# Kernel optimization log

Measured on AMD Instinct MI355X. Metric: run time of the kernel, lower is better.

## Reference

```python
import jax, jax.numpy as jnp
import numpy as np
from math import factorial, sqrt

LMAX = 2
NB = 32
NRBF = 20
CUTOFF = 5.0
N_ATOMS = 20000
N_EDGES = 400000
T = 2
M = (LMAX + 1) ** 2
LIDX = np.repeat(np.arange(LMAX + 1), 2 * np.arange(LMAX + 1) + 1)  # l of each flat (l,m) index


def _cg_complex(j1, m1, j2, m2, j3, m3):
    # Racah formula for complex-SH Clebsch-Gordan coefficients
    if m3 != m1 + m2 or j3 < abs(j1 - j2) or j3 > j1 + j2:
        return 0.0
    f = factorial
    pref = sqrt((2 * j3 + 1) * f(j1 + j2 - j3) * f(j1 - j2 + j3) * f(-j1 + j2 + j3) / f(j1 + j2 + j3 + 1))
    pref *= sqrt(f(j1 + m1) * f(j1 - m1) * f(j2 + m2) * f(j2 - m2) * f(j3 + m3) * f(j3 - m3))
    kmin = max(0, j2 - j3 - m1, j1 + m2 - j3)
    kmax = min(j1 + j2 - j3, j1 - m1, j2 + m2)
    s = 0.0
    for k in range(kmin, kmax + 1):
        s += (-1) ** k / (f(k) * f(j1 + j2 - j3 - k) * f(j1 - m1 - k) * f(j2 + m2 - k) * f(j3 - j2 + m1 + k) * f(j3 - j1 - m2 + k))
    return pref * s


def _u_matrix(l):
    # real-SH = U @ complex-SH (rows: real m from -l..l, cols: complex m')
    U = np.zeros((2 * l + 1, 2 * l + 1), dtype=np.complex128)
    for m in range(-l, l + 1):
        if m == 0:
            U[l, l] = 1.0
        elif m > 0:
            U[l + m, l + m] = (-1) ** m / sqrt(2)
            U[l + m, l - m] = 1.0 / sqrt(2)
        else:
            mu = -m
            U[l + m, l + m] = 1j / sqrt(2)
            U[l + m, l - m] = -1j * (-1) ** mu / sqrt(2)
    return U


def _build_cg_rsh(lmax):
    # CG coefficients in the real-SH basis, parity invariant (odd l1+l2+l3 blocks zero)
    cg = np.zeros((M, M, M), dtype=np.float64)
    Us = [_u_matrix(l) for l in range(lmax + 1)]
    for l1 in range(lmax + 1):
        for l2 in range(lmax + 1):
            for l3 in range(lmax + 1):
                if (l1 + l2 + l3) % 2 == 1 or l3 < abs(l1 - l2) or l3 > l1 + l2:
                    continue
                Cc = np.zeros((2 * l1 + 1, 2 * l2 + 1, 2 * l3 + 1), dtype=np.complex128)
                for i, m1 in enumerate(range(-l1, l1 + 1)):
                    for j, m2 in enumerate(range(-l2, l2 + 1)):
                        m3 = m1 + m2
                        if abs(m3) <= l3:
                            Cc[i, j, l3 + m3] = _cg_complex(l1, m1, l2, m2, l3, m3)
                R = np.einsum('ai,bj,ck,ijk->abc', Us[l1], Us[l2], np.conj(Us[l3]), Cc)
                cg[l1 * l1:(l1 + 1) ** 2, l2 * l2:(l2 + 1) ** 2, l3 * l3:(l3 + 1) ** 2] = np.real(R)
    return cg.astype(np.float32)


CG = jnp.asarray(_build_cg_rsh(LMAX))   # [9, 9, 9]
LIDX_J = jnp.asarray(LIDX)


def _rsh(dirs):
    # real spherical harmonics up to l=2 on unit vectors, flat (l,m) order -> [P, 9]
    x, y, z = dirs[:, 0], dirs[:, 1], dirs[:, 2]
    c1 = 0.4886025119029199
    c2 = 1.0925484305920792
    return jnp.stack([
        jnp.full_like(x, 0.28209479177387814),
        c1 * y, c1 * z, c1 * x,
        c2 * x * y, c2 * y * z,
        0.31539156525252005 * (3.0 * z * z - 1.0),
        c2 * x * z,
        0.5462742152960396 * (x * x - y * y),
    ], axis=1)


def _forward(atomic_numbers, r_ij, idx_i, idx_j, emb, Wf, bf, Wm1, Wm2, Wm3, Wg, bg):
    d = jnp.linalg.norm(r_ij, axis=1)                      # [P]
    Y = _rsh(r_ij / d[:, None])                            # [P, 9]
    offsets = jnp.linspace(0.0, CUTOFF, NRBF)
    width = CUTOFF / (NRBF - 1)
    radial = jnp.exp(-0.5 / width ** 2 * (d[:, None] - offsets) ** 2)   # GaussianRBF [P, NRBF]
    fcut = jnp.where(d < CUTOFF, 0.5 * (jnp.cos(d * jnp.pi / CUTOFF) + 1.0), 0.0)  # CosineCutoff
    x0 = emb[atomic_numbers]                               # nuclear embedding [N, NB]
    x = jnp.concatenate([x0[:, None, :], jnp.zeros((x0.shape[0], M - 1, NB), x0.dtype)], axis=1)  # scalar2rsh
    for t in range(T):
        # SO3Convolution: per-edge radial filter per output degree l, cutoff gated
        Wl = ((radial @ Wf[t].T + bf[t]) * fcut[:, None]).reshape(-1, LMAX + 1, NB)
        xj = x[idx_j]                                      # gather neighbors [P, 9, NB]
        tbc = jnp.einsum('pa,abc->pbc', Y, CG)             # contract Y_ij with CG
        yij = jnp.einsum('pbc,pbn->pcn', tbc, xj) * Wl[:, LIDX_J, :]
        dx = jax.ops.segment_sum(yij, idx_i, num_segments=x.shape[0], indices_are_sorted=True)
        ddx = jnp.einsum('xcn,kn->xck', dx, Wm1[t])        # mixing1 (no bias)
        dx = dx + jnp.einsum('abc,xan,xbn->xcn', CG, dx, ddx)  # SO3TensorProduct
        dx = jnp.einsum('xcn,kn->xck', dx, Wm2[t])         # mixing2
        h = jax.nn.sigmoid((dx[:, 0, :] @ Wg[t].T + bg[t]).reshape(-1, LMAX + 1, NB))
        dx = dx * h[:, LIDX_J, :]                          # SO3ParametricGatedNonlinearity
        dx = jnp.einsum('xcn,kn->xck', dx, Wm3[t])         # mixing3
        x = x + dx
    return x                                               # multipole representation [N, 9, NB]


def setup_inputs():
    key = jax.random.key(0)
    ks = jax.random.split(key, 12)
    return {
        'atomic_numbers': jax.random.randint(ks[0], (N_ATOMS,), 1, 100),
        'r_ij': jax.random.normal(ks[1], (N_EDGES, 3), jnp.float32),
        'idx_i': jnp.sort(jax.random.randint(ks[2], (N_EDGES,), 0, N_ATOMS)),
        'idx_j': jax.random.randint(ks[3], (N_EDGES,), 0, N_ATOMS),
        'emb': jax.random.normal(ks[4], (101, NB), jnp.float32).at[0].set(0.0),
        'Wf': jax.random.normal(ks[5], (T, (LMAX + 1) * NB, NRBF), jnp.float32) / sqrt(NRBF),
        'bf': jnp.zeros((T, (LMAX + 1) * NB), jnp.float32),
        'Wm1': jax.random.normal(ks[6], (T, NB, NB), jnp.float32) / sqrt(NB),
        'Wm2': jax.random.normal(ks[7], (T, NB, NB), jnp.float32) / sqrt(NB),
        'Wm3': jax.random.normal(ks[8], (T, NB, NB), jnp.float32) / sqrt(NB),
        'Wg': jax.random.normal(ks[9], (T, (LMAX + 1) * NB, NB), jnp.float32) / sqrt(NB),
        'bg': jnp.zeros((T, (LMAX + 1) * NB), jnp.float32),
    }


def reference(atomic_numbers, r_ij, idx_i, idx_j, emb, Wf, bf, Wm1, Wm2, Wm3, Wg, bg):
    return _forward(atomic_numbers, r_ij, idx_i, idx_j, emb, Wf, bf, Wm1, Wm2, Wm3, Wg, bg)
```

## Files before the change

### kernel.cpp

```cpp
#include <hip/hip_runtime.h>

#define CHUNK 16

constexpr double CFACT[8] = {1.,1.,2.,6.,24.,120.,720.,5040.};

constexpr double csqrt(double x){
  if (x <= 0.0) return 0.0;
  double s = 1.0;
  while (x > 4.0)  { x *= 0.25; s *= 2.0; }
  while (x < 0.25) { x *= 4.0;  s *= 0.5; }
  double g = 1.0;
  for (int i=0;i<10;i++) g = 0.5*(g + x/g);
  return s*g;
}

constexpr double cg_complex(int j1,int m1,int j2,int m2,int j3,int m3){
  if (m3 != m1+m2 || j3 < (j1>j2?j1-j2:j2-j1) || j3 > j1+j2) return 0.0;
  double pref = csqrt((2.0*j3+1.0)*CFACT[j1+j2-j3]*CFACT[j1-j2+j3]*CFACT[-j1+j2+j3]/CFACT[j1+j2+j3+1]);
  pref *= csqrt(CFACT[j1+m1]*CFACT[j1-m1]*CFACT[j2+m2]*CFACT[j2-m2]*CFACT[j3+m3]*CFACT[j3-m3]);
  int kmin = 0;
  if (j2-j3-m1 > kmin) kmin = j2-j3-m1;
  if (j1+m2-j3 > kmin) kmin = j1+m2-j3;
  int kmax = j1+j2-j3;
  if (j1-m1 < kmax) kmax = j1-m1;
  if (j2+m2 < kmax) kmax = j2+m2;
  double s = 0.0;
  for (int k=kmin;k<=kmax;++k){
    double t = 1.0/(CFACT[k]*CFACT[j1+j2-j3-k]*CFACT[j1-m1-k]*CFACT[j2+m2-k]*CFACT[j3-j2+m1+k]*CFACT[j3-j1-m2+k]);
    s += (k&1)? -t : t;
  }
  return pref*s;
}

struct UR { int n; int mc[2]; double re[2]; double im[2]; };
constexpr UR u_row(int m){
  UR u{}; const double is2 = 0.70710678118654752440;
  if (m==0){ u.n=1; u.mc[0]=0; u.re[0]=1.0; u.im[0]=0.0; u.mc[1]=0; u.re[1]=0.0; u.im[1]=0.0; }
  else if (m>0){ u.n=2; u.mc[0]=m;  u.re[0]=((m&1)? -is2:is2); u.im[0]=0.0;
                        u.mc[1]=-m; u.re[1]=is2;               u.im[1]=0.0; }
  else { int mu=-m; u.n=2; u.mc[0]=m;  u.re[0]=0.0; u.im[0]=is2;
                           u.mc[1]=mu; u.re[1]=0.0; u.im[1]=((mu&1)? is2:-is2); }
  return u;
}

struct CGTab { float v[9][9][9]; };
constexpr CGTab build_cg(){
  CGTab g{};
  double cc[9][9][9] = {};
  for (int a=0;a<9;a++){
    int l1 = (a==0)?0:((a<4)?1:2); int m1 = a - (l1*l1+l1);
    for (int b=0;b<9;b++){
      int l2 = (b==0)?0:((b<4)?1:2); int m2 = b - (l2*l2+l2);
      int m3 = m1+m2;
      for (int l3=0;l3<=2;l3++){
        if (m3 < -l3 || m3 > l3) continue;
        cc[a][b][l3*l3+l3+m3] = cg_complex(l1,m1,l2,m2,l3,m3);
      }
    }
  }
  for (int l1=0;l1<=2;l1++) for (int l2=0;l2<=2;l2++) for (int l3=0;l3<=2;l3++){
    if (((l1+l2+l3)&1)==1) continue;
    int dl = (l1>l2)?(l1-l2):(l2-l1);
    if (l3 < dl || l3 > l1+l2) continue;
    for (int m1=-l1;m1<=l1;m1++) for (int m2=-l2;m2<=l2;m2++) for (int m3=-l3;m3<=l3;m3++){
      UR ua = u_row(m1), ub = u_row(m2), uc = u_row(m3);
      double acc = 0.0;
      for (int i=0;i<ua.n;i++) for (int j=0;j<ub.n;j++){
        double zr = ua.re[i]*ub.re[j] - ua.im[i]*ub.im[j];
        double zi = ua.re[i]*ub.im[j] + ua.im[i]*ub.re[j];
        for (int k=0;k<uc.n;k++){
          double rp = zr*uc.re[k] + zi*uc.im[k];
          if (rp != 0.0)
            acc += rp * cc[l1*l1+l1+ua.mc[i]][l2*l2+l2+ub.mc[j]][l3*l3+l3+uc.mc[k]];
        }
      }
      g.v[l1*l1+l1+m1][l2*l2+l2+m2][l3*l3+l3+m3] = (float)acc;
    }
  }
  return g;
}
constexpr CGTab CGT = build_cg();

__device__ __forceinline__ int swizzle_block(int b, int nb){
  int P = nb >> 3;
  if (b < (P<<3)) return (b & 7) * P + (b >> 3);
  return b;
}

template<bool FIRST>
__global__ __launch_bounds__(256) void edge_kernel(
    const float* __restrict__ r_ij, const int* __restrict__ idx_i, const int* __restrict__ idx_j,
    const float* __restrict__ x, const int* __restrict__ Z, const float* __restrict__ emb,
    const float* __restrict__ Wf_t, const float* __restrict__ bf_t,
    float* __restrict__ dx, int n_edges)
{
  int tid = threadIdx.x;
  int g = tid >> 5, lane = tid & 31;

  int vb = swizzle_block(blockIdx.x, gridDim.x);
  int base = (vb*8 + g)*CHUNK;
  if (base >= n_edges) return;

  int pidx;
  {
    int e0 = base + (lane & 15);
    if (e0 > n_edges-1) e0 = n_edges-1;
    pidx = (lane < 16) ? idx_i[e0] : idx_j[e0];
  }
  float rv0, rv1;
  {
    long long rmax = (long long)n_edges*3 - 1;
    long long a0 = (long long)base*3 + lane;       if (a0 > rmax) a0 = rmax;
    long long a1 = (long long)base*3 + 32 + lane;  if (a1 > rmax) a1 = rmax;
    rv0 = r_ij[a0];
    rv1 = r_ij[a1];
  }

  float wfr[3][20]; float bfl[3];
  #pragma unroll
  for (int l=0;l<3;l++){
    const float* rp = Wf_t + (l*32+lane)*20;
    #pragma unroll
    for (int q=0;q<5;q++){
      float4 v4 = *reinterpret_cast<const float4*>(rp + q*4);
      wfr[l][q*4+0]=v4.x; wfr[l][q*4+1]=v4.y; wfr[l][q*4+2]=v4.z; wfr[l][q*4+3]=v4.w;
    }
    bfl[l] = bf_t[l*32+lane];
  }

  const float STEP  = 5.0f/19.0f;
  const float ALPHA = -0.5f/(STEP*STEP);
  float myoff = (float)lane * STEP;

  float racc[9];
  #pragma unroll
  for (int c=0;c<9;c++) racc[c]=0.f;
  int cur_i = -1;

  float xjn[9]; float xjn0;
  {
    int j0 = __shfl(pidx, 16, 32);
    if (FIRST){
      xjn0 = emb[Z[j0]*32 + lane];
    } else {
      const float* xp = x + j0*288 + lane;
      #pragma unroll
      for (int b=0;b<9;b++) xjn[b] = xp[b*32];
    }
  }

  #pragma unroll
  for (int k=0;k<CHUNK;k++){
    int e = base + k;
    if (e >= n_edges) break;

    float xj[9]; float xj0;
    if (FIRST){
      xj0 = xjn0;
    } else {
      #pragma unroll
      for (int b=0;b<9;b++) xj[b] = xjn[b];
    }

    if (k+1 < CHUNK){
      int jn = __shfl(pidx, 16+k+1, 32);
      if (FIRST){
        xjn0 = emb[Z[jn]*32 + lane];
      } else {
        const float* xp = x + jn*288 + lane;
        #pragma unroll
        for (int b=0;b<9;b++) xjn[b] = xp[b*32];
      }
    }

    int ii = __shfl(pidx, k, 32);

    float rx = (3*k+0 < 32) ? __shfl(rv0, 3*k+0, 32) : __shfl(rv1, 3*k+0-32, 32);
    float ry = (3*k+1 < 32) ? __shfl(rv0, 3*k+1, 32) : __shfl(rv1, 3*k+1-32, 32);
    float rz = (3*k+2 < 32) ? __shfl(rv0, 3*k+2, 32) : __shfl(rv1, 3*k+2-32, 32);

    float d2 = fmaf(rx,rx,fmaf(ry,ry,rz*rz));
    float dd = sqrtf(d2);
    float inv = __fdividef(1.0f, dd);
    float X = rx*inv, Yv = ry*inv, Zv = rz*inv;
    const float c1 = 0.4886025119029199f, c2 = 1.0925484305920792f;
    float Y[9];
    Y[0]=0.28209479177387814f; Y[1]=c1*Yv; Y[2]=c1*Zv; Y[3]=c1*X;
    Y[4]=c2*X*Yv; Y[5]=c2*Yv*Zv; Y[6]=0.31539156525252005f*(3.f*Zv*Zv-1.f);
    Y[7]=c2*X*Zv; Y[8]=0.5462742152960396f*(X*X-Yv*Yv);

    float dtl = dd - myoff;
    float rbl = __expf(ALPHA*dtl*dtl);
    float wl0=bfl[0], wl1=bfl[1], wl2=bfl[2];
    #pragma unroll
    for (int r=0;r<20;r++){
      float rb = __shfl(rbl, r, 32);
      wl0 = fmaf(rb, wfr[0][r], wl0);
      wl1 = fmaf(rb, wfr[1][r], wl1);
      wl2 = fmaf(rb, wfr[2][r], wl2);
    }
    float fc = (dd < 5.0f) ? 0.5f*(__cosf(dd*0.6283185307179586f)+1.0f) : 0.0f;
    wl0*=fc; wl1*=fc; wl2*=fc;

    if (ii != cur_i){
      if (cur_i >= 0){
        float* dp = dx + cur_i*288 + lane;
        #pragma unroll
        for (int c=0;c<9;c++){ atomicAdd(dp + c*32, racc[c]); racc[c]=0.f; }
      }
      cur_i = ii;
    }

    if (FIRST){
      racc[0] = fmaf(wl0, Y[0]*xj0, racc[0]);
      #pragma unroll
      for (int c=1;c<4;c++) racc[c] = fmaf(wl1, Y[c]*xj0, racc[c]);
      #pragma unroll
      for (int c=4;c<9;c++) racc[c] = fmaf(wl2, Y[c]*xj0, racc[c]);
    } else {
      float yv[9];
      #pragma unroll
      for (int c=0;c<9;c++) yv[c]=0.f;
      #pragma unroll
      for (int a=0;a<9;a++){
        #pragma unroll
        for (int b=0;b<9;b++){
          bool any = false;
          #pragma unroll
          for (int c=0;c<9;c++) any = any | (CGT.v[a][b][c] != 0.f);
          if (any){
            float p = Y[a]*xj[b];
            #pragma unroll
            for (int c=0;c<9;c++){
              if (CGT.v[a][b][c] != 0.f) yv[c] = fmaf(CGT.v[a][b][c], p, yv[c]);
            }
          }
        }
      }
      racc[0] = fmaf(wl0, yv[0], racc[0]);
      #pragma unroll
      for (int c=1;c<4;c++) racc[c] = fmaf(wl1, yv[c], racc[c]);
      #pragma unroll
      for (int c=4;c<9;c++) racc[c] = fmaf(wl2, yv[c], racc[c]);
    }
  }
  if (cur_i >= 0){
    float* dp = dx + cur_i*288 + lane;
    #pragma unroll
    for (int c=0;c<9;c++) atomicAdd(dp + c*32, racc[c]);
  }
}

template<bool FIRST, bool LAST>
__global__ __launch_bounds__(256) void atom_kernel(
    float* __restrict__ x, float* __restrict__ dxg,
    const int* __restrict__ Z, const float* __restrict__ emb,
    const float* __restrict__ Wm1_t, const float* __restrict__ Wm2_t, const float* __restrict__ Wm3_t,
    const float* __restrict__ Wg_t, const float* __restrict__ bg_t, int n_atoms)
{
  __shared__ __align__(16) float tile[8][288];
  int tid = threadIdx.x;
  int g = tid>>5, k = tid&31;
  int vb = swizzle_block(blockIdx.x, gridDim.x);
  int atom = vb*8 + g;
  if (atom >= n_atoms) return;
  float* tg = &tile[g][0];
  const float4* t4 = reinterpret_cast<const float4*>(tg);

  float embv;
  if (FIRST) embv = emb[Z[atom]*32 + k];

  float* dp = dxg + atom*288 + k;
  float v[9];
  #pragma unroll
  for (int c=0;c<9;c++){
    v[c]=dp[c*32]; tg[c*32+k]=v[c];
    if (!LAST) dp[c*32]=0.f;
  }

  float wr[32];
  {
    const float4* w4 = reinterpret_cast<const float4*>(Wm1_t + k*32);
    #pragma unroll
    for (int q=0;q<8;q++){ float4 a=w4[q]; wr[4*q]=a.x; wr[4*q+1]=a.y; wr[4*q+2]=a.z; wr[4*q+3]=a.w; }
  }
  float u[9];
  #pragma unroll
  for (int c=0;c<9;c++){
    float s=0.f;
    #pragma unroll
    for (int q=0;q<8;q++){
      float4 tv = t4[c*8+q];
      s = fmaf(tv.x, wr[4*q+0], s); s = fmaf(tv.y, wr[4*q+1], s);
      s = fmaf(tv.z, wr[4*q+2], s); s = fmaf(tv.w, wr[4*q+3], s);
    }
    u[c]=s;
  }

  float w[9];
  #pragma unroll
  for (int c=0;c<9;c++) w[c]=v[c];
  #pragma unroll
  for (int a=0;a<9;a++){
    #pragma unroll
    for (int b=0;b<9;b++){
      bool any = false;
      #pragma unroll
      for (int c=0;c<9;c++) any = any | (CGT.v[a][b][c] != 0.f);
      if (any){
        float p = v[a]*u[b];
        #pragma unroll
        for (int c=0;c<9;c++){
          if (CGT.v[a][b][c] != 0.f) w[c] = fmaf(CGT.v[a][b][c], p, w[c]);
        }
      }
    }
  }

  #pragma unroll
  for (int c=0;c<9;c++) tg[c*32+k]=w[c];
  {
    const float4* w4 = reinterpret_cast<const float4*>(Wm2_t + k*32);
    #pragma unroll
    for (int q=0;q<8;q++){ float4 a=w4[q]; wr[4*q]=a.x; wr[4*q+1]=a.y; wr[4*q+2]=a.z; wr[4*q+3]=a.w; }
  }
  float p[9];
  #pragma unroll
  for (int c=0;c<9;c++){
    float s=0.f;
    #pragma unroll
    for (int q=0;q<8;q++){
      float4 tv = t4[c*8+q];
      s = fmaf(tv.x, wr[4*q+0], s); s = fmaf(tv.y, wr[4*q+1], s);
      s = fmaf(tv.z, wr[4*q+2], s); s = fmaf(tv.w, wr[4*q+3], s);
    }
    p[c]=s;
  }

  tg[k] = p[0];
  float s0=bg_t[k], s1=bg_t[32+k], s2=bg_t[64+k];
  {
    const float4* wg0 = reinterpret_cast<const float4*>(Wg_t + (     k)*32);
    const float4* wg1 = reinterpret_cast<const float4*>(Wg_t + (32 + k)*32);
    const float4* wg2 = reinterpret_cast<const float4*>(Wg_t + (64 + k)*32);
    #pragma unroll
    for (int q=0;q<8;q++){
      float4 tv = t4[q];
      float4 a0 = wg0[q], a1 = wg1[q], a2 = wg2[q];
      s0 = fmaf(tv.x,a0.x,s0); s0 = fmaf(tv.y,a0.y,s0); s0 = fmaf(tv.z,a0.z,s0); s0 = fmaf(tv.w,a0.w,s0);
      s1 = fmaf(tv.x,a1.x,s1); s1 = fmaf(tv.y,a1.y,s1); s1 = fmaf(tv.z,a1.z,s1); s1 = fmaf(tv.w,a1.w,s1);
      s2 = fmaf(tv.x,a2.x,s2); s2 = fmaf(tv.y,a2.y,s2); s2 = fmaf(tv.z,a2.z,s2); s2 = fmaf(tv.w,a2.w,s2);
    }
  }
  float h0 = 1.f/(1.f+__expf(-s0));
  float h1 = 1.f/(1.f+__expf(-s1));
  float h2 = 1.f/(1.f+__expf(-s2));

  float q9[9];
  q9[0]=p[0]*h0;
  #pragma unroll
  for (int c=1;c<4;c++) q9[c]=p[c]*h1;
  #pragma unroll
  for (int c=4;c<9;c++) q9[c]=p[c]*h2;

  #pragma unroll
  for (int c=0;c<9;c++) tg[c*32+k]=q9[c];
  {
    const float4* w4 = reinterpret_cast<const float4*>(Wm3_t + k*32);
    #pragma unroll
    for (int q=0;q<8;q++){ float4 a=w4[q]; wr[4*q]=a.x; wr[4*q+1]=a.y; wr[4*q+2]=a.z; wr[4*q+3]=a.w; }
  }
  float* xo = x + atom*288 + k;
  #pragma unroll
  for (int c=0;c<9;c++){
    float s=0.f;
    #pragma unroll
    for (int q=0;q<8;q++){
      float4 tv = t4[c*8+q];
      s = fmaf(tv.x, wr[4*q+0], s); s = fmaf(tv.y, wr[4*q+1], s);
      s = fmaf(tv.z, wr[4*q+2], s); s = fmaf(tv.w, wr[4*q+3], s);
    }
    if (FIRST){
      float base = (c==0)? embv : 0.f;
      xo[c*32] = base + s;
    } else {
      xo[c*32] += s;
    }
  }
}

extern "C" void kernel_launch(void* const* d_in, const int* in_sizes, int n_in,
                              void* d_out, int out_size, void* d_ws, size_t ws_size,
                              hipStream_t stream)
{
  const int*   Z    = (const int*)d_in[0];
  const float* r_ij = (const float*)d_in[1];
  const int*   idxi = (const int*)d_in[2];
  const int*   idxj = (const int*)d_in[3];
  const float* emb  = (const float*)d_in[4];
  const float* Wf   = (const float*)d_in[5];
  const float* bf   = (const float*)d_in[6];
  const float* Wm1  = (const float*)d_in[7];
  const float* Wm2  = (const float*)d_in[8];
  const float* Wm3  = (const float*)d_in[9];
  const float* Wg   = (const float*)d_in[10];
  const float* bg   = (const float*)d_in[11];
  int n_atoms = in_sizes[0];
  int n_edges = in_sizes[1]/3;

  float* x  = (float*)d_out;
  float* dx = (float*)d_ws;

  hipMemsetAsync(dx, 0, (size_t)n_atoms*288*sizeof(float), stream);

  int eblocks = (n_edges + 8*CHUNK - 1)/(8*CHUNK);
  int ablocks = (n_atoms + 7)/8;

  edge_kernel<true><<<eblocks,256,0,stream>>>(r_ij, idxi, idxj, x, Z, emb, Wf, bf, dx, n_edges);
  atom_kernel<true,false><<<ablocks,256,0,stream>>>(x, dx, Z, emb, Wm1, Wm2, Wm3, Wg, bg, n_atoms);

  edge_kernel<false><<<eblocks,256,0,stream>>>(r_ij, idxi, idxj, x, Z, emb,
                                        Wf + 96*20, bf + 96, dx, n_edges);
  atom_kernel<false,true><<<ablocks,256,0,stream>>>(x, dx, Z, emb,
                                        Wm1 + 1024, Wm2 + 1024, Wm3 + 1024,
                                        Wg + 96*32, bg + 96, n_atoms);
}
```

Before: 428.9 us.

## Fuse all passes into one persistent kernel with software grid barriers

Merges the memset, both edge passes and both atom passes into a single persistent kernel sized by occupancy. Blocks loop over edge groups and atoms with grid-stride loops and synchronize between phases via atomic-counter grid barriers. This removes kernel launch gaps and the separate memset. In exchange it adds spin-barrier cost, drops the block swizzle, and may raise register pressure and lower occupancy, since one kernel holds every phase.

New measurement: 779.2 us. 81.7% more time.

```diff
diff --git a/kernel.cpp b/kernel.cpp
--- a/kernel.cpp
+++ b/kernel.cpp
@@ -81,14 +81,19 @@
 }
 constexpr CGTab CGT = build_cg();
 
-__device__ __forceinline__ int swizzle_block(int b, int nb){
-  int P = nb >> 3;
-  if (b < (P<<3)) return (b & 7) * P + (b >> 3);
-  return b;
+__device__ __forceinline__ void grid_barrier(int* cnt, int idx, int nblocks){
+  __threadfence();
+  __syncthreads();
+  if (threadIdx.x == 0){
+    atomicAdd(&cnt[idx], 1);
+    while (atomicAdd(&cnt[idx], 0) < nblocks) __builtin_amdgcn_s_sleep(2);
+  }
+  __syncthreads();
+  __threadfence();
 }
 
 template<bool FIRST>
-__global__ __launch_bounds__(256) void edge_kernel(
+__device__ void edge_phase(
     const float* __restrict__ r_ij, const int* __restrict__ idx_i, const int* __restrict__ idx_j,
     const float* __restrict__ x, const int* __restrict__ Z, const float* __restrict__ emb,
     const float* __restrict__ Wf_t, const float* __restrict__ bf_t,
@@ -97,25 +102,6 @@
   int tid = threadIdx.x;
   int g = tid >> 5, lane = tid & 31;
 
-  int vb = swizzle_block(blockIdx.x, gridDim.x);
-  int base = (vb*8 + g)*CHUNK;
-  if (base >= n_edges) return;
-
-  int pidx;
-  {
-    int e0 = base + (lane & 15);
-    if (e0 > n_edges-1) e0 = n_edges-1;
-    pidx = (lane < 16) ? idx_i[e0] : idx_j[e0];
-  }
-  float rv0, rv1;
-  {
-    long long rmax = (long long)n_edges*3 - 1;
-    long long a0 = (long long)base*3 + lane;       if (a0 > rmax) a0 = rmax;
-    long long a1 = (long long)base*3 + 32 + lane;  if (a1 > rmax) a1 = rmax;
-    rv0 = r_ij[a0];
-    rv1 = r_ij[a1];
-  }
-
   float wfr[3][20]; float bfl[3];
   #pragma unroll
   for (int l=0;l<3;l++){
@@ -132,261 +118,312 @@
   const float ALPHA = -0.5f/(STEP*STEP);
   float myoff = (float)lane * STEP;
 
-  float racc[9];
-  #pragma unroll
-  for (int c=0;c<9;c++) racc[c]=0.f;
-  int cur_i = -1;
-
-  float xjn[9]; float xjn0;
-  {
-    int j0 = __shfl(pidx, 16, 32);
-    if (FIRST){
-      xjn0 = emb[Z[j0]*32 + lane];
-    } else {
-      const float* xp = x + j0*288 + lane;
-      #pragma unroll
-      for (int b=0;b<9;b++) xjn[b] = xp[b*32];
-    }
-  }
-
-  #pragma unroll
-  for (int k=0;k<CHUNK;k++){
-    int e = base + k;
-    if (e >= n_edges) break;
-
-    float xj[9]; float xj0;
-    if (FIRST){
-      xj0 = xjn0;
-    } else {
-      #pragma unroll
-      for (int b=0;b<9;b++) xj[b] = xjn[b];
-    }
-
-    if (k+1 < CHUNK){
-      int jn = __shfl(pidx, 16+k+1, 32);
+  const int ngroups = (n_edges + CHUNK - 1)/CHUNK;
+
+  for (int grp = blockIdx.x*8 + g; grp < ngroups; grp += gridDim.x*8){
+    int base = grp*CHUNK;
+
+    int pidx;
+    {
+      int e0 = base + (lane & 15);
+      if (e0 > n_edges-1) e0 = n_edges-1;
+      pidx = (lane < 16) ? idx_i[e0] : idx_j[e0];
+    }
+    float rv0, rv1;
+    {
+      long long rmax = (long long)n_edges*3 - 1;
+      long long a0 = (long long)base*3 + lane;       if (a0 > rmax) a0 = rmax;
+      long long a1 = (long long)base*3 + 32 + lane;  if (a1 > rmax) a1 = rmax;
+      rv0 = r_ij[a0];
+      rv1 = r_ij[a1];
+    }
+
+    float racc[9];
+    #pragma unroll
+    for (int c=0;c<9;c++) racc[c]=0.f;
+    int cur_i = -1;
+
+    float xjn[9]; float xjn0;
+    {
+      int j0 = __shfl(pidx, 16, 32);
       if (FIRST){
-        xjn0 = emb[Z[jn]*32 + lane];
+        xjn0 = emb[Z[j0]*32 + lane];
       } else {
-        const float* xp = x + jn*288 + lane;
+        const float* xp = x + j0*288 + lane;
         #pragma unroll
         for (int b=0;b<9;b++) xjn[b] = xp[b*32];
       }
     }
 
-    int ii = __shfl(pidx, k, 32);
-
-    float rx = (3*k+0 < 32) ? __shfl(rv0, 3*k+0, 32) : __shfl(rv1, 3*k+0-32, 32);
-    float ry = (3*k+1 < 32) ? __shfl(rv0, 3*k+1, 32) : __shfl(rv1, 3*k+1-32, 32);
-    float rz = (3*k+2 < 32) ? __shfl(rv0, 3*k+2, 32) : __shfl(rv1, 3*k+2-32, 32);
-
-    float d2 = fmaf(rx,rx,fmaf(ry,ry,rz*rz));
-    float dd = sqrtf(d2);
-    float inv = __fdividef(1.0f, dd);
-    float X = rx*inv, Yv = ry*inv, Zv = rz*inv;
-    const float c1 = 0.4886025119029199f, c2 = 1.0925484305920792f;
-    float Y[9];
-    Y[0]=0.28209479177387814f; Y[1]=c1*Yv; Y[2]=c1*Zv; Y[3]=c1*X;
-    Y[4]=c2*X*Yv; Y[5]=c2*Yv*Zv; Y[6]=0.31539156525252005f*(3.f*Zv*Zv-1.f);
-    Y[7]=c2*X*Zv; Y[8]=0.5462742152960396f*(X*X-Yv*Yv);
-
-    float dtl = dd - myoff;
-    float rbl = __expf(ALPHA*dtl*dtl);
-    float wl0=bfl[0], wl1=bfl[1], wl2=bfl[2];
-    #pragma unroll
-    for (int r=0;r<20;r++){
-      float rb = __shfl(rbl, r, 32);
-      wl0 = fmaf(rb, wfr[0][r], wl0);
-      wl1 = fmaf(rb, wfr[1][r], wl1);
-      wl2 = fmaf(rb, wfr[2][r], wl2);
-    }
-    float fc = (dd < 5.0f) ? 0.5f*(__cosf(dd*0.6283185307179586f)+1.0f) : 0.0f;
-    wl0*=fc; wl1*=fc; wl2*=fc;
-
-    if (ii != cur_i){
-      if (cur_i >= 0){
-        float* dp = dx + cur_i*288 + lane;
-        #pragma unroll
-        for (int c=0;c<9;c++){ atomicAdd(dp + c*32, racc[c]); racc[c]=0.f; }
-      }
-      cur_i = ii;
-    }
-
-    if (FIRST){
-      racc[0] = fmaf(wl0, Y[0]*xj0, racc[0]);
-      #pragma unroll
-      for (int c=1;c<4;c++) racc[c] = fmaf(wl1, Y[c]*xj0, racc[c]);
-      #pragma unroll
-      for (int c=4;c<9;c++) racc[c] = fmaf(wl2, Y[c]*xj0, racc[c]);
-    } else {
-      float yv[9];
-      #pragma unroll
-      for (int c=0;c<9;c++) yv[c]=0.f;
-      #pragma unroll
-      for (int a=0;a<9;a++){
-        #pragma unroll
-        for (int b=0;b<9;b++){
-          bool any = false;
+    #pragma unroll
+    for (int k=0;k<CHUNK;k++){
+      int e = base + k;
+      if (e >= n_edges) break;
+
+      float xj[9]; float xj0;
+      if (FIRST){
+        xj0 = xjn0;
+      } else {
+        #pragma unroll
+        for (int b=0;b<9;b++) xj[b] = xjn[b];
+      }
+
+      if (k+1 < CHUNK){
+        int jn = __shfl(pidx, 16+k+1, 32);
+        if (FIRST){
+          xjn0 = emb[Z[jn]*32 + lane];
+        } else {
+          const float* xp = x + jn*288 + lane;
           #pragma unroll
-          for (int c=0;c<9;c++) any = any | (CGT.v[a][b][c] != 0.f);
-          if (any){
-            float p = Y[a]*xj[b];
+          for (int b=0;b<9;b++) xjn[b] = xp[b*32];
+        }
+      }
+
+      int ii = __shfl(pidx, k, 32);
+
+      float rx = (3*k+0 < 32) ? __shfl(rv0, 3*k+0, 32) : __shfl(rv1, 3*k+0-32, 32);
+      float ry = (3*k+1 < 32) ? __shfl(rv0, 3*k+1, 32) : __shfl(rv1, 3*k+1-32, 32);
+      float rz = (3*k+2 < 32) ? __shfl(rv0, 3*k+2, 32) : __shfl(rv1, 3*k+2-32, 32);
+
+      float d2 = fmaf(rx,rx,fmaf(ry,ry,rz*rz));
+      float dd = sqrtf(d2);
+      float inv = __fdividef(1.0f, dd);
+      float X = rx*inv, Yv = ry*inv, Zv = rz*inv;
+      const float c1 = 0.4886025119029199f, c2 = 1.0925484305920792f;
+      float Y[9];
+      Y[0]=0.28209479177387814f; Y[1]=c1*Yv; Y[2]=c1*Zv; Y[3]=c1*X;
+      Y[4]=c2*X*Yv; Y[5]=c2*Yv*Zv; Y[6]=0.31539156525252005f*(3.f*Zv*Zv-1.f);
+      Y[7]=c2*X*Zv; Y[8]=0.5462742152960396f*(X*X-Yv*Yv);
+
+      float dtl = dd - myoff;
+      float rbl = __expf(ALPHA*dtl*dtl);
+      float wl0=bfl[0], wl1=bfl[1], wl2=bfl[2];
+      #pragma unroll
+      for (int r=0;r<20;r++){
+        float rb = __shfl(rbl, r, 32);
+        wl0 = fmaf(rb, wfr[0][r], wl0);
+        wl1 = fmaf(rb, wfr[1][r], wl1);
+        wl2 = fmaf(rb, wfr[2][r], wl2);
+      }
+      float fc = (dd < 5.0f) ? 0.5f*(__cosf(dd*0.6283185307179586f)+1.0f) : 0.0f;
+      wl0*=fc; wl1*=fc; wl2*=fc;
+
+      if (ii != cur_i){
+        if (cur_i >= 0){
+          float* dp = dx + cur_i*288 + lane;
+          #pragma unroll
+          for (int c=0;c<9;c++){ atomicAdd(dp + c*32, racc[c]); racc[c]=0.f; }
+        }
+        cur_i = ii;
+      }
+
+      if (FIRST){
+        racc[0] = fmaf(wl0, Y[0]*xj0, racc[0]);
+        #pragma unroll
+        for (int c=1;c<4;c++) racc[c] = fmaf(wl1, Y[c]*xj0, racc[c]);
+        #pragma unroll
+        for (int c=4;c<9;c++) racc[c] = fmaf(wl2, Y[c]*xj0, racc[c]);
+      } else {
+        float yv[9];
+        #pragma unroll
+        for (int c=0;c<9;c++) yv[c]=0.f;
+        #pragma unroll
+        for (int a=0;a<9;a++){
+          #pragma unroll
+          for (int b=0;b<9;b++){
+            bool any = false;
             #pragma unroll
-            for (int c=0;c<9;c++){
-              if (CGT.v[a][b][c] != 0.f) yv[c] = fmaf(CGT.v[a][b][c], p, yv[c]);
+            for (int c=0;c<9;c++) any = any | (CGT.v[a][b][c] != 0.f);
+            if (any){
+              float p = Y[a]*xj[b];
+              #pragma unroll
+              for (int c=0;c<9;c++){
+                if (CGT.v[a][b][c] != 0.f) yv[c] = fmaf(CGT.v[a][b][c], p, yv[c]);
+              }
             }
           }
         }
-      }
-      racc[0] = fmaf(wl0, yv[0], racc[0]);
-      #pragma unroll
-      for (int c=1;c<4;c++) racc[c] = fmaf(wl1, yv[c], racc[c]);
-      #pragma unroll
-      for (int c=4;c<9;c++) racc[c] = fmaf(wl2, yv[c], racc[c]);
-    }
-  }
-  if (cur_i >= 0){
-    float* dp = dx + cur_i*288 + lane;
-    #pragma unroll
-    for (int c=0;c<9;c++) atomicAdd(dp + c*32, racc[c]);
+        racc[0] = fmaf(wl0, yv[0], racc[0]);
+        #pragma unroll
+        for (int c=1;c<4;c++) racc[c] = fmaf(wl1, yv[c], racc[c]);
+        #pragma unroll
+        for (int c=4;c<9;c++) racc[c] = fmaf(wl2, yv[c], racc[c]);
+      }
+    }
+    if (cur_i >= 0){
+      float* dp = dx + cur_i*288 + lane;
+      #pragma unroll
+      for (int c=0;c<9;c++) atomicAdd(dp + c*32, racc[c]);
+    }
   }
 }
 
 template<bool FIRST, bool LAST>
-__global__ __launch_bounds__(256) void atom_kernel(
+__device__ void atom_phase(
     float* __restrict__ x, float* __restrict__ dxg,
     const int* __restrict__ Z, const float* __restrict__ emb,
     const float* __restrict__ Wm1_t, const float* __restrict__ Wm2_t, const float* __restrict__ Wm3_t,
-    const float* __restrict__ Wg_t, const float* __restrict__ bg_t, int n_atoms)
+    const float* __restrict__ Wg_t, const float* __restrict__ bg_t, int n_atoms,
+    float* tile)
 {
-  __shared__ __align__(16) float tile[8][288];
   int tid = threadIdx.x;
   int g = tid>>5, k = tid&31;
-  int vb = swizzle_block(blockIdx.x, gridDim.x);
-  int atom = vb*8 + g;
-  if (atom >= n_atoms) return;
-  float* tg = &tile[g][0];
+  float* tg = tile + g*288;
   const float4* t4 = reinterpret_cast<const float4*>(tg);
 
-  float embv;
-  if (FIRST) embv = emb[Z[atom]*32 + k];
-
-  float* dp = dxg + atom*288 + k;
-  float v[9];
-  #pragma unroll
-  for (int c=0;c<9;c++){
-    v[c]=dp[c*32]; tg[c*32+k]=v[c];
-    if (!LAST) dp[c*32]=0.f;
-  }
-
-  float wr[32];
+  for (int atom = blockIdx.x*8 + g; atom < n_atoms; atom += gridDim.x*8){
+    float embv;
+    if (FIRST) embv = emb[Z[atom]*32 + k];
+
+    float* dp = dxg + atom*288 + k;
+    float v[9];
+    #pragma unroll
+    for (int c=0;c<9;c++){
+      v[c]=dp[c*32]; tg[c*32+k]=v[c];
+      if (!LAST) dp[c*32]=0.f;
+    }
+
+    float wr[32];
+    {
+      const float4* w4 = reinterpret_cast<const float4*>(Wm1_t + k*32);
+      #pragma unroll
+      for (int q=0;q<8;q++){ float4 a=w4[q]; wr[4*q]=a.x; wr[4*q+1]=a.y; wr[4*q+2]=a.z; wr[4*q+3]=a.w; }
+    }
+    float u[9];
+    #pragma unroll
+    for (int c=0;c<9;c++){
+      float s=0.f;
+      #pragma unroll
+      for (int q=0;q<8;q++){
+        float4 tv = t4[c*8+q];
+        s = fmaf(tv.x, wr[4*q+0], s); s = fmaf(tv.y, wr[4*q+1], s);
+        s = fmaf(tv.z, wr[4*q+2], s); s = fmaf(tv.w, wr[4*q+3], s);
+      }
+      u[c]=s;
+    }
+
+    float w[9];
+    #pragma unroll
+    for (int c=0;c<9;c++) w[c]=v[c];
+    #pragma unroll
+    for (int a=0;a<9;a++){
+      #pragma unroll
+      for (int b=0;b<9;b++){
+        bool any = false;
+        #pragma unroll
+        for (int c=0;c<9;c++) any = any | (CGT.v[a][b][c] != 0.f);
+        if (any){
+          float p = v[a]*u[b];
+          #pragma unroll
+          for (int c=0;c<9;c++){
+            if (CGT.v[a][b][c] != 0.f) w[c] = fmaf(CGT.v[a][b][c], p, w[c]);
+          }
+        }
+      }
+    }
+
+    #pragma unroll
+    for (int c=0;c<9;c++) tg[c*32+k]=w[c];
+    {
+      const float4* w4 = reinterpret_cast<const float4*>(Wm2_t + k*32);
+      #pragma unroll
+      for (int q=0;q<8;q++){ float4 a=w4[q]; wr[4*q]=a.x; wr[4*q+1]=a.y; wr[4*q+2]=a.z; wr[4*q+3]=a.w; }
+    }
+    float p[9];
+    #pragma unroll
+    for (int c=0;c<9;c++){
+      float s=0.f;
+      #pragma unroll
+      for (int q=0;q<8;q++){
+        float4 tv = t4[c*8+q];
+        s = fmaf(tv.x, wr[4*q+0], s); s = fmaf(tv.y, wr[4*q+1], s);
+        s = fmaf(tv.z, wr[4*q+2], s); s = fmaf(tv.w, wr[4*q+3], s);
+      }
+      p[c]=s;
+    }
+
+    tg[k] = p[0];
+    float s0=bg_t[k], s1=bg_t[32+k], s2=bg_t[64+k];
+    {
+      const float4* wg0 = reinterpret_cast<const float4*>(Wg_t + (     k)*32);
+      const float4* wg1 = reinterpret_cast<const float4*>(Wg_t + (32 + k)*32);
+      const float4* wg2 = reinterpret_cast<const float4*>(Wg_t + (64 + k)*32);
+      #pragma unroll
+      for (int q=0;q<8;q++){
+        float4 tv = t4[q];
+        float4 a0 = wg0[q], a1 = wg1[q], a2 = wg2[q];
+        s0 = fmaf(tv.x,a0.x,s0); s0 = fmaf(tv.y,a0.y,s0); s0 = fmaf(tv.z,a0.z,s0); s0 = fmaf(tv.w,a0.w,s0);
+        s1 = fmaf(tv.x,a1.x,s1); s1 = fmaf(tv.y,a1.y,s1); s1 = fmaf(tv.z,a1.z,s1); s1 = fmaf(tv.w,a1.w,s1);
+        s2 = fmaf(tv.x,a2.x,s2); s2 = fmaf(tv.y,a2.y,s2); s2 = fmaf(tv.z,a2.z,s2); s2 = fmaf(tv.w,a2.w,s2);
+      }
+    }
+    float h0 = 1.f/(1.f+__expf(-s0));
+    float h1 = 1.f/(1.f+__expf(-s1));
+    float h2 = 1.f/(1.f+__expf(-s2));
+
+    float q9[9];
+    q9[0]=p[0]*h0;
+    #pragma unroll
+    for (int c=1;c<4;c++) q9[c]=p[c]*h1;
+    #pragma unroll
+    for (int c=4;c<9;c++) q9[c]=p[c]*h2;
+
+    #pragma unroll
+    for (int c=0;c<9;c++) tg[c*32+k]=q9[c];
+    {
+      const float4* w4 = reinterpret_cast<const float4*>(Wm3_t + k*32);
+      #pragma unroll
+      for (int q=0;q<8;q++){ float4 a=w4[q]; wr[4*q]=a.x; wr[4*q+1]=a.y; wr[4*q+2]=a.z; wr[4*q+3]=a.w; }
+    }
+    float* xo = x + atom*288 + k;
+    #pragma unroll
+    for (int c=0;c<9;c++){
+      float s=0.f;
+      #pragma unroll
+      for (int q=0;q<8;q++){
+        float4 tv = t4[c*8+q];
+        s = fmaf(tv.x, wr[4*q+0], s); s = fmaf(tv.y, wr[4*q+1], s);
+        s = fmaf(tv.z, wr[4*q+2], s); s = fmaf(tv.w, wr[4*q+3], s);
+      }
+      if (FIRST){
+        float base = (c==0)? embv : 0.f;
+        xo[c*32] = base + s;
+      } else {
+        xo[c*32] += s;
+      }
+    }
+  }
+}
+
+__global__ __launch_bounds__(256) void fused_kernel(
+    const float* __restrict__ r_ij, const int* __restrict__ idx_i, const int* __restrict__ idx_j,
+    const int* __restrict__ Z, const float* __restrict__ emb,
+    const float* __restrict__ Wf, const float* __restrict__ bf,
+    const float* __restrict__ Wm1, const float* __restrict__ Wm2, const float* __restrict__ Wm3,
+    const float* __restrict__ Wg, const float* __restrict__ bg,
+    float* __restrict__ x, float* __restrict__ dx, int* __restrict__ cnt,
+    int n_atoms, int n_edges, int nblocks)
+{
+  __shared__ __align__(16) float tile[8*288];
+  int tid = threadIdx.x;
+
   {
-    const float4* w4 = reinterpret_cast<const float4*>(Wm1_t + k*32);
-    #pragma unroll
-    for (int q=0;q<8;q++){ float4 a=w4[q]; wr[4*q]=a.x; wr[4*q+1]=a.y; wr[4*q+2]=a.z; wr[4*q+3]=a.w; }
-  }
-  float u[9];
-  #pragma unroll
-  for (int c=0;c<9;c++){
-    float s=0.f;
-    #pragma unroll
-    for (int q=0;q<8;q++){
-      float4 tv = t4[c*8+q];
-      s = fmaf(tv.x, wr[4*q+0], s); s = fmaf(tv.y, wr[4*q+1], s);
-      s = fmaf(tv.z, wr[4*q+2], s); s = fmaf(tv.w, wr[4*q+3], s);
-    }
-    u[c]=s;
-  }
-
-  float w[9];
-  #pragma unroll
-  for (int c=0;c<9;c++) w[c]=v[c];
-  #pragma unroll
-  for (int a=0;a<9;a++){
-    #pragma unroll
-    for (int b=0;b<9;b++){
-      bool any = false;
-      #pragma unroll
-      for (int c=0;c<9;c++) any = any | (CGT.v[a][b][c] != 0.f);
-      if (any){
-        float p = v[a]*u[b];
-        #pragma unroll
-        for (int c=0;c<9;c++){
-          if (CGT.v[a][b][c] != 0.f) w[c] = fmaf(CGT.v[a][b][c], p, w[c]);
-        }
-      }
-    }
-  }
-
-  #pragma unroll
-  for (int c=0;c<9;c++) tg[c*32+k]=w[c];
-  {
-    const float4* w4 = reinterpret_cast<const float4*>(Wm2_t + k*32);
-    #pragma unroll
-    for (int q=0;q<8;q++){ float4 a=w4[q]; wr[4*q]=a.x; wr[4*q+1]=a.y; wr[4*q+2]=a.z; wr[4*q+3]=a.w; }
-  }
-  float p[9];
-  #pragma unroll
-  for (int c=0;c<9;c++){
-    float s=0.f;
-    #pragma unroll
-    for (int q=0;q<8;q++){
-      float4 tv = t4[c*8+q];
-      s = fmaf(tv.x, wr[4*q+0], s); s = fmaf(tv.y, wr[4*q+1], s);
-      s = fmaf(tv.z, wr[4*q+2], s); s = fmaf(tv.w, wr[4*q+3], s);
-    }
-    p[c]=s;
-  }
-
-  tg[k] = p[0];
-  float s0=bg_t[k], s1=bg_t[32+k], s2=bg_t[64+k];
-  {
-    const float4* wg0 = reinterpret_cast<const float4*>(Wg_t + (     k)*32);
-    const float4* wg1 = reinterpret_cast<const float4*>(Wg_t + (32 + k)*32);
-    const float4* wg2 = reinterpret_cast<const float4*>(Wg_t + (64 + k)*32);
-    #pragma unroll
-    for (int q=0;q<8;q++){
-      float4 tv = t4[q];
-      float4 a0 = wg0[q], a1 = wg1[q], a2 = wg2[q];
-      s0 = fmaf(tv.x,a0.x,s0); s0 = fmaf(tv.y,a0.y,s0); s0 = fmaf(tv.z,a0.z,s0); s0 = fmaf(tv.w,a0.w,s0);
-      s1 = fmaf(tv.x,a1.x,s1); s1 = fmaf(tv.y,a1.y,s1); s1 = fmaf(tv.z,a1.z,s1); s1 = fmaf(tv.w,a1.w,s1);
-      s2 = fmaf(tv.x,a2.x,s2); s2 = fmaf(tv.y,a2.y,s2); s2 = fmaf(tv.z,a2.z,s2); s2 = fmaf(tv.w,a2.w,s2);
-    }
-  }
-  float h0 = 1.f/(1.f+__expf(-s0));
-  float h1 = 1.f/(1.f+__expf(-s1));
-  float h2 = 1.f/(1.f+__expf(-s2));
-
-  float q9[9];
-  q9[0]=p[0]*h0;
-  #pragma unroll
-  for (int c=1;c<4;c++) q9[c]=p[c]*h1;
-  #pragma unroll
-  for (int c=4;c<9;c++) q9[c]=p[c]*h2;
-
-  #pragma unroll
-  for (int c=0;c<9;c++) tg[c*32+k]=q9[c];
-  {
-    const float4* w4 = reinterpret_cast<const float4*>(Wm3_t + k*32);
-    #pragma unroll
-    for (int q=0;q<8;q++){ float4 a=w4[q]; wr[4*q]=a.x; wr[4*q+1]=a.y; wr[4*q+2]=a.z; wr[4*q+3]=a.w; }
-  }
-  float* xo = x + atom*288 + k;
-  #pragma unroll
-  for (int c=0;c<9;c++){
-    float s=0.f;
-    #pragma unroll
-    for (int q=0;q<8;q++){
-      float4 tv = t4[c*8+q];
-      s = fmaf(tv.x, wr[4*q+0], s); s = fmaf(tv.y, wr[4*q+1], s);
-      s = fmaf(tv.z, wr[4*q+2], s); s = fmaf(tv.w, wr[4*q+3], s);
-    }
-    if (FIRST){
-      float base = (c==0)? embv : 0.f;
-      xo[c*32] = base + s;
-    } else {
-      xo[c*32] += s;
-    }
-  }
+    int n4 = n_atoms*72;
+    float4* dx4 = reinterpret_cast<float4*>(dx);
+    float4 z = make_float4(0.f,0.f,0.f,0.f);
+    for (int i = blockIdx.x*256 + tid; i < n4; i += gridDim.x*256) dx4[i] = z;
+  }
+  grid_barrier(cnt, 0, nblocks);
+
+  edge_phase<true>(r_ij, idx_i, idx_j, x, Z, emb, Wf, bf, dx, n_edges);
+  grid_barrier(cnt, 1, nblocks);
+  atom_phase<true,false>(x, dx, Z, emb, Wm1, Wm2, Wm3, Wg, bg, n_atoms, tile);
+  grid_barrier(cnt, 2, nblocks);
+
+  edge_phase<false>(r_ij, idx_i, idx_j, x, Z, emb, Wf + 96*20, bf + 96, dx, n_edges);
+  grid_barrier(cnt, 3, nblocks);
+  atom_phase<false,true>(x, dx, Z, emb, Wm1 + 1024, Wm2 + 1024, Wm3 + 1024,
+                         Wg + 96*32, bg + 96, n_atoms, tile);
 }
 
 extern "C" void kernel_launch(void* const* d_in, const int* in_sizes, int n_in,
@@ -408,20 +445,22 @@
   int n_atoms = in_sizes[0];
   int n_edges = in_sizes[1]/3;
 
-  float* x  = (float*)d_out;
-  float* dx = (float*)d_ws;
-
-  hipMemsetAsync(dx, 0, (size_t)n_atoms*288*sizeof(float), stream);
-
-  int eblocks = (n_edges + 8*CHUNK - 1)/(8*CHUNK);
-  int ablocks = (n_atoms + 7)/8;
-
-  edge_kernel<true><<<eblocks,256,0,stream>>>(r_ij, idxi, idxj, x, Z, emb, Wf, bf, dx, n_edges);
-  atom_kernel<true,false><<<ablocks,256,0,stream>>>(x, dx, Z, emb, Wm1, Wm2, Wm3, Wg, bg, n_atoms);
-
-  edge_kernel<false><<<eblocks,256,0,stream>>>(r_ij, idxi, idxj, x, Z, emb,
-                                        Wf + 96*20, bf + 96, dx, n_edges);
-  atom_kernel<false,true><<<ablocks,256,0,stream>>>(x, dx, Z, emb,
-                                        Wm1 + 1024, Wm2 + 1024, Wm3 + 1024,
-                                        Wg + 96*32, bg + 96, n_atoms);
-}
+  float* x   = (float*)d_out;
+  int*   cnt = (int*)d_ws;
+  float* dx  = (float*)((char*)d_ws + 256);
+
+  int occ = 0, ncu = 0;
+  (void)hipOccupancyMaxActiveBlocksPerMultiprocessor(&occ, (const void*)fused_kernel, 256, 0);
+  (void)hipDeviceGetAttribute(&ncu, hipDeviceAttributeMultiprocessorCount, 0);
+  if (occ < 1) occ = 1;
+  if (ncu < 1) ncu = 256;
+  long long G = (long long)occ * ncu;
+  long long maxwork = ((n_edges + CHUNK - 1)/CHUNK + 7)/8;
+  if (G > maxwork) G = maxwork;
+  if (G < 1) G = 1;
+
+  hipMemsetAsync(cnt, 0, 256, stream);
+  fused_kernel<<<(int)G, 256, 0, stream>>>(r_ij, idxi, idxj, Z, emb,
+                                           Wf, bf, Wm1, Wm2, Wm3, Wg, bg,
+                                           x, dx, cnt, n_atoms, n_edges, (int)G);
+}
```
